# Kernel tuning notes

Hardware: AMD Instinct MI355X
Metric: run time of the kernel (lower is better)

## Reference

```python
import jax, jax.numpy as jnp
import numpy as np

# Thresholds from PointsGeneration.__init__ defaults
THRES_TEXT = 0.45
THRES_HEAD = 0.5
THRES_BOND = 0.5

H = W = 2048


def setup_inputs() -> dict:
    key = jax.random.key(0)
    ks = jax.random.split(key, 7)
    mk = lambda k, c: jax.random.normal(k, (1, c, H, W), dtype=jnp.float32)
    return {
        "score_text": mk(ks[0], 1),
        "score_head": mk(ks[1], 1),
        "score_tail": mk(ks[2], 1),
        "score_bond": mk(ks[3], 1),
        "reg_head": mk(ks[4], 4),
        "reg_tail": mk(ks[5], 4),
        "reg_bond": mk(ks[6], 4),
    }


def reference(score_text, score_head, score_tail, score_bond, reg_head, reg_tail, reg_bond):
    # Sigmoid activations (exactly as in torch forward).
    s_text = jax.nn.sigmoid(score_text)
    s_head = jax.nn.sigmoid(score_head)
    s_tail = jax.nn.sigmoid(score_tail)
    s_bond = jax.nn.sigmoid(score_bond)

    # Per-pixel thresholding performed by the .so before per-instance point
    # generation: center-text mask, head/tail masks (within text region),
    # pixels passing the corresponding mask, so we gate them here.
    m_text = (s_text > THRES_TEXT).astype(s_text.dtype)   # [1,1,H,W]
    m_head = m_text * (s_head > THRES_HEAD).astype(s_head.dtype)
    m_tail = m_text * (s_tail > THRES_HEAD).astype(s_tail.dtype)
    m_bond = (s_bond > THRES_BOND).astype(s_bond.dtype)

    gated = jnp.concatenate([
        reg_head * m_head,   # [1,4,H,W]
        reg_tail * m_tail,   # [1,4,H,W]
        reg_bond * m_bond,   # [1,4,H,W]
    ], axis=1)

    return jnp.concatenate([s_text, s_head, s_tail, s_bond, gated], axis=1)
```

## Files before the change

### kernel.cpp

```cpp
#include <hip/hip_runtime.h>
#include <math.h>


typedef float f32x4 __attribute__((ext_vector_type(4)));
typedef unsigned long long u64;

static __device__ __forceinline__ float sigf(float x) {
    return 1.0f / (1.0f + expf(-x));
}

static __device__ __forceinline__ f32x4 ld4(const float* p) {
    return *reinterpret_cast<const f32x4*>(p);
}
static __device__ __forceinline__ void st4(float* p, f32x4 v) {
    *reinterpret_cast<f32x4*>(p) = v;
}

static __device__ __forceinline__ u64 score_plane(
    const float* __restrict__ src, float* __restrict__ dst,
    float thr, int base)
{
    f32x4 V[16];
#pragma unroll
    for (int j = 0; j < 16; ++j) V[j] = ld4(src + base + j * 256);
    u64 m = 0;
#pragma unroll
    for (int j = 0; j < 16; ++j) {
#pragma unroll
        for (int k = 0; k < 4; ++k) {
            V[j][k] = sigf(V[j][k]);
            if (V[j][k] > thr) m |= 1ull << (4 * j + k);
        }
    }
#pragma unroll
    for (int j = 0; j < 16; ++j) st4(dst + base + j * 256, V[j]);
    return m;
}

static __device__ __forceinline__ void reg_plane(
    const float* __restrict__ src, float* __restrict__ dst,
    u64 m, int base)
{
    f32x4 V[16];
#pragma unroll
    for (int j = 0; j < 16; ++j) V[j] = ld4(src + base + j * 256);
#pragma unroll
    for (int j = 0; j < 16; ++j) {
#pragma unroll
        for (int k = 0; k < 4; ++k) {
            V[j][k] = ((m >> (4 * j + k)) & 1ull) ? V[j][k] : 0.0f;
        }
    }
#pragma unroll
    for (int j = 0; j < 16; ++j) st4(dst + base + j * 256, V[j]);
}

__global__ __launch_bounds__(256) void points_gen_kernel(
    const float* __restrict__ p_text,
    const float* __restrict__ p_head,
    const float* __restrict__ p_tail,
    const float* __restrict__ p_bond,
    const float* __restrict__ p_rh,
    const float* __restrict__ p_rt,
    const float* __restrict__ p_rb,
    float* __restrict__ out)
{
    constexpr int N = 2048 * 2048;
    constexpr int WPX = 4096;
    const int lane = threadIdx.x & 63;
    const int wave = (blockIdx.x * blockDim.x + threadIdx.x) >> 6;
    const int base = wave * WPX + lane * 4;

    const u64 mt = score_plane(p_text, out + 0 * N, 0.45f, base);
    const u64 mh = score_plane(p_head, out + 1 * N, 0.50f, base) & mt;
    const u64 ml = score_plane(p_tail, out + 2 * N, 0.50f, base) & mt;
    const u64 mb = score_plane(p_bond, out + 3 * N, 0.50f, base);

#pragma unroll
    for (int c = 0; c < 4; ++c)
        reg_plane(p_rh + c * N, out + (4 + c) * N, mh, base);
#pragma unroll
    for (int c = 0; c < 4; ++c)
        reg_plane(p_rt + c * N, out + (8 + c) * N, ml, base);
#pragma unroll
    for (int c = 0; c < 4; ++c)
        reg_plane(p_rb + c * N, out + (12 + c) * N, mb, base);
}

extern "C" void kernel_launch(void* const* d_in, const int* in_sizes, int n_in,
                              void* d_out, int out_size, void* d_ws, size_t ws_size,
                              hipStream_t stream) {
    (void)in_sizes; (void)n_in; (void)out_size; (void)d_ws; (void)ws_size;

    const float* p_text = (const float*)d_in[0];
    const float* p_head = (const float*)d_in[1];
    const float* p_tail = (const float*)d_in[2];
    const float* p_bond = (const float*)d_in[3];
    const float* p_rh   = (const float*)d_in[4];
    const float* p_rt   = (const float*)d_in[5];
    const float* p_rb   = (const float*)d_in[6];
    float* out = (float*)d_out;

    constexpr int N = 2048 * 2048;
    constexpr int WPX = 4096;
    constexpr int waves = N / WPX;
    constexpr int threads = 256;
    constexpr int blocks = waves * 64 / threads;

    points_gen_kernel<<<blocks, threads, 0, stream>>>(
        p_text, p_head, p_tail, p_bond, p_rh, p_rt, p_rb, out);
}
```

Before: 113.5 us.

## Split work per pixel window across four specialized waves with recomputed masks

Each 2048-pixel window is now handled by four waves in one block. One wave writes the four sigmoid planes, and each of the other three builds its own mask and gates one group of regression planes. The goal is more parallelism and smaller per-wave register footprints (8 vectors instead of 16, 32-bit masks), for more occupancy and memory-level parallelism. In exchange, score planes are re-read and sigmoids recomputed for the masks. The text plane is loaded three times per window, mostly expected to hit cache.

```diff
diff --git a/kernel.cpp b/kernel.cpp
--- a/kernel.cpp
+++ b/kernel.cpp
@@ -3,7 +3,6 @@
 
 
 typedef float f32x4 __attribute__((ext_vector_type(4)));
-typedef unsigned long long u64;
 
 static __device__ __forceinline__ float sigf(float x) {
     return 1.0f / (1.0f + expf(-x));
@@ -16,43 +15,49 @@
     *reinterpret_cast<f32x4*>(p) = v;
 }
 
-static __device__ __forceinline__ u64 score_plane(
-    const float* __restrict__ src, float* __restrict__ dst,
-    float thr, int base)
+static __device__ __forceinline__ void plane_sig(
+    const float* __restrict__ src, float* __restrict__ dst, int base)
 {
-    f32x4 V[16];
+    f32x4 v[8];
 #pragma unroll
-    for (int j = 0; j < 16; ++j) V[j] = ld4(src + base + j * 256);
-    u64 m = 0;
+    for (int j = 0; j < 8; ++j) v[j] = ld4(src + base + j * 256);
 #pragma unroll
-    for (int j = 0; j < 16; ++j) {
+    for (int j = 0; j < 8; ++j)
 #pragma unroll
-        for (int k = 0; k < 4; ++k) {
-            V[j][k] = sigf(V[j][k]);
-            if (V[j][k] > thr) m |= 1ull << (4 * j + k);
-        }
-    }
+        for (int k = 0; k < 4; ++k) v[j][k] = sigf(v[j][k]);
 #pragma unroll
-    for (int j = 0; j < 16; ++j) st4(dst + base + j * 256, V[j]);
+    for (int j = 0; j < 8; ++j) st4(dst + base + j * 256, v[j]);
+}
+
+static __device__ __forceinline__ unsigned mask_of(
+    const float* __restrict__ src, float thr, int base)
+{
+    f32x4 v[8];
+#pragma unroll
+    for (int j = 0; j < 8; ++j) v[j] = ld4(src + base + j * 256);
+    unsigned m = 0;
+#pragma unroll
+    for (int j = 0; j < 8; ++j)
+#pragma unroll
+        for (int k = 0; k < 4; ++k)
+            if (sigf(v[j][k]) > thr) m |= 1u << (4 * j + k);
     return m;
 }
 
-static __device__ __forceinline__ void reg_plane(
+static __device__ __forceinline__ void gate(
     const float* __restrict__ src, float* __restrict__ dst,
-    u64 m, int base)
+    unsigned m, int base)
 {
-    f32x4 V[16];
+    f32x4 v[8];
 #pragma unroll
-    for (int j = 0; j < 16; ++j) V[j] = ld4(src + base + j * 256);
+    for (int j = 0; j < 8; ++j) v[j] = ld4(src + base + j * 256);
 #pragma unroll
-    for (int j = 0; j < 16; ++j) {
+    for (int j = 0; j < 8; ++j)
 #pragma unroll
-        for (int k = 0; k < 4; ++k) {
-            V[j][k] = ((m >> (4 * j + k)) & 1ull) ? V[j][k] : 0.0f;
-        }
-    }
+        for (int k = 0; k < 4; ++k)
+            v[j][k] = ((m >> (4 * j + k)) & 1u) ? v[j][k] : 0.0f;
 #pragma unroll
-    for (int j = 0; j < 16; ++j) st4(dst + base + j * 256, V[j]);
+    for (int j = 0; j < 8; ++j) st4(dst + base + j * 256, v[j]);
 }
 
 __global__ __launch_bounds__(256) void points_gen_kernel(
@@ -66,25 +71,36 @@
     float* __restrict__ out)
 {
     constexpr int N = 2048 * 2048;
-    constexpr int WPX = 4096;
+    constexpr int WPX = 2048;
     const int lane = threadIdx.x & 63;
-    const int wave = (blockIdx.x * blockDim.x + threadIdx.x) >> 6;
-    const int base = wave * WPX + lane * 4;
+    const int gwave = blockIdx.x * 4 + (threadIdx.x >> 6);
+    const int g = gwave & 3;
+    const int w = gwave >> 2;
+    const int base = w * WPX + lane * 4;
 
-    const u64 mt = score_plane(p_text, out + 0 * N, 0.45f, base);
-    const u64 mh = score_plane(p_head, out + 1 * N, 0.50f, base) & mt;
-    const u64 ml = score_plane(p_tail, out + 2 * N, 0.50f, base) & mt;
-    const u64 mb = score_plane(p_bond, out + 3 * N, 0.50f, base);
-
+    if (g == 0) {
+        plane_sig(p_text, out + 0 * N, base);
+        plane_sig(p_head, out + 1 * N, base);
+        plane_sig(p_tail, out + 2 * N, base);
+        plane_sig(p_bond, out + 3 * N, base);
+    } else if (g == 1) {
+        const unsigned m = mask_of(p_text, 0.45f, base) &
+                           mask_of(p_head, 0.50f, base);
 #pragma unroll
-    for (int c = 0; c < 4; ++c)
-        reg_plane(p_rh + c * N, out + (4 + c) * N, mh, base);
+        for (int c = 0; c < 4; ++c)
+            gate(p_rh + c * N, out + (4 + c) * N, m, base);
+    } else if (g == 2) {
+        const unsigned m = mask_of(p_text, 0.45f, base) &
+                           mask_of(p_tail, 0.50f, base);
 #pragma unroll
-    for (int c = 0; c < 4; ++c)
-        reg_plane(p_rt + c * N, out + (8 + c) * N, ml, base);
+        for (int c = 0; c < 4; ++c)
+            gate(p_rt + c * N, out + (8 + c) * N, m, base);
+    } else {
+        const unsigned m = mask_of(p_bond, 0.50f, base);
 #pragma unroll
-    for (int c = 0; c < 4; ++c)
-        reg_plane(p_rb + c * N, out + (12 + c) * N, mb, base);
+        for (int c = 0; c < 4; ++c)
+            gate(p_rb + c * N, out + (12 + c) * N, m, base);
+    }
 }
 
 extern "C" void kernel_launch(void* const* d_in, const int* in_sizes, int n_in,
@@ -102,11 +118,11 @@
     float* out = (float*)d_out;
 
     constexpr int N = 2048 * 2048;
-    constexpr int WPX = 4096;
-    constexpr int waves = N / WPX;
-    constexpr int threads = 256;
-    constexpr int blocks = waves * 64 / threads;
+    constexpr int WPX = 2048;
+    constexpr int windows = N / WPX;
+    constexpr int waves = windows * 4;
+    constexpr int blocks = waves / 4;
 
-    points_gen_kernel<<<blocks, threads, 0, stream>>>(
+    points_gen_kernel<<<blocks, 256, 0, stream>>>(
         p_text, p_head, p_tail, p_bond, p_rh, p_rt, p_rb, out);
 }
```

After: 106.8 us (median of 2 runs). -5.9%, faster.
